# Kernel tuning notes

Hardware: AMD Instinct MI355X
Metric: run time of the kernel (lower is better)

Reference implementation:

```python
import jax, jax.numpy as jnp
import numpy as np

N_HEADS = 16
LN_EPS = 1e-5


def _layer_norm(x, g, b):
    mu = jnp.mean(x, axis=-1, keepdims=True)
    var = jnp.mean(jnp.square(x - mu), axis=-1, keepdims=True)
    return (x - mu) * jax.lax.rsqrt(var + LN_EPS) * g + b


def setup_inputs() -> dict:
    key = jax.random.key(0)
    ks = jax.random.split(key, 6)
    B, S, D = 2, 2048, 1024
    d_ff = 4 * D
    sc = lambda fan_in: 1.0 / np.sqrt(fan_in)
    return {
        "x": jax.random.normal(ks[0], (B, S, D), jnp.float32),
        "in_proj_w": jax.random.normal(ks[1], (3 * D, D), jnp.float32) * sc(D),
        "in_proj_b": jnp.zeros((3 * D,), jnp.float32),
        "out_proj_w": jax.random.normal(ks[2], (D, D), jnp.float32) * sc(D),
        "out_proj_b": jnp.zeros((D,), jnp.float32),
        "ln1_g": jnp.ones((D,), jnp.float32),
        "ln1_b": jnp.zeros((D,), jnp.float32),
        "w1": jax.random.normal(ks[3], (d_ff, D), jnp.float32) * sc(D),
        "b1": jnp.zeros((d_ff,), jnp.float32),
        "w2": jax.random.normal(ks[4], (D, d_ff), jnp.float32) * sc(d_ff),
        "b2": jnp.zeros((D,), jnp.float32),
        "ln2_g": jnp.ones((D,), jnp.float32),
        "ln2_b": jnp.zeros((D,), jnp.float32),
        "window": 128,
    }


def reference(x, in_proj_w, in_proj_b, out_proj_w, out_proj_b,
              ln1_g, ln1_b, w1, b1, w2, b2, ln2_g, ln2_b, window):
    B, S, D = x.shape
    H = N_HEADS
    hd = D // H

    # fused QKV projection (torch Linear convention: x @ W.T + b)
    qkv = x @ in_proj_w.T + in_proj_b            # (B, S, 3D)
    q, k, v = jnp.split(qkv, 3, axis=-1)
    to_heads = lambda t: t.reshape(B, S, H, hd).transpose(0, 2, 1, 3)  # (B,H,S,hd)
    q, k, v = to_heads(q), to_heads(k), to_heads(v)

    scores = jnp.einsum("bhqd,bhkd->bhqk", q, k) / jnp.sqrt(jnp.asarray(hd, x.dtype))
    # banded mask: position i attends to j with |i - j| <= window
    idx = jnp.arange(S)
    band = jnp.abs(idx[:, None] - idx[None, :]) <= window   # (S, S) bool
    scores = jnp.where(band, scores, -jnp.inf)
    probs = jax.nn.softmax(scores, axis=-1)

    attn = jnp.einsum("bhqk,bhkd->bhqd", probs, v)           # (B,H,S,hd)
    attn = attn.transpose(0, 2, 1, 3).reshape(B, S, D)
    attn_out = attn @ out_proj_w.T + out_proj_b

    x2 = _layer_norm(x + attn_out, ln1_g, ln1_b)
    ff = jax.nn.relu(x2 @ w1.T + b1) @ w2.T + b2
    x3 = _layer_norm(x2 + ff, ln2_g, ln2_b)
    return x3
```

## Files before the change

### kernel.cpp

```cpp
#include <hip/hip_runtime.h>
#include <hip/hip_bf16.h>

#define AS1 __attribute__((address_space(1)))
#define AS3 __attribute__((address_space(3)))

typedef __bf16 bf16x8_t __attribute__((ext_vector_type(8)));
typedef float f32x4_t __attribute__((ext_vector_type(4)));
typedef unsigned short ushort_t;
typedef unsigned int uint_t;

static __device__ __forceinline__ ushort_t f2b(float f) {
    __hip_bfloat16 h = __float2bfloat16(f);
    return __builtin_bit_cast(unsigned short, h);
}
static __device__ __forceinline__ float b2f(ushort_t u) {
    return __uint_as_float((uint_t)u << 16);
}

struct CastArgs {
    const float* src[5];
    ushort_t* dst[5];
    int cum[6];
};

__global__ __launch_bounds__(256) void cast_all(CastArgs a) {
    const int i = blockIdx.x * 256 + threadIdx.x;
    if (i >= a.cum[5]) return;
    int s = 0;
#pragma unroll
    for (int k = 1; k < 5; ++k) s += (i >= a.cum[k]);
    const int idx = i - a.cum[s];
    float4 v = ((const float4*)a.src[s])[idx];
    ushort4 o;
    o.x = f2b(v.x); o.y = f2b(v.y); o.z = f2b(v.z); o.w = f2b(v.w);
    ((ushort4*)a.dst[s])[idx] = o;
}

#define EPI_BIAS 1
#define EPI_RELU 2
#define EPI_PART 8
#define EPI_OUTB 16

struct PB { ushort_t* p[4]; };

template <int F>
__global__ __launch_bounds__(256, 2) void gemm_bt(const ushort_t* __restrict__ A,
                                                  const ushort_t* __restrict__ B,
                                                  const float* __restrict__ bias,
                                                  PB pb,
                                                  ushort_t* __restrict__ outb,
                                                  int M, int N, int Kc, int ld) {
    __shared__ ushort_t la[128 * 64];
    __shared__ ushort_t lb[128 * 64];
    const int t = threadIdx.x;

    const int nx = gridDim.x, ny = gridDim.y, nz = gridDim.z;
    const int lid = blockIdx.x + nx * (blockIdx.y + ny * blockIdx.z);
    const int xcd = lid & 7;
    const int slot = lid >> 3;
    const int n_i = slot % nx;
    const int rest = slot / nx;
    const int z = rest % nz;
    const int m_i = xcd * (ny >> 3) + rest / nz;

    const int n0 = n_i * 128;
    const int m0 = m_i * 128;
    const int k0 = z * Kc;
    const int lane = t & 63;
    const int w = t >> 6;
    const int wr = w >> 1, wc = w & 1;
    const int r16 = lane & 15, kq = lane >> 4;

    f32x4_t acc[4][4] = {};

    size_t aoff[4], boff[4];
#pragma unroll
    for (int p = 0; p < 4; ++p) {
        const int c = t + 256 * p;
        const int row = c >> 3, cc = c & 7;
        const int gcol = (cc ^ (row & 7)) * 8;
        aoff[p] = (size_t)(m0 + row) * ld + gcol + k0;
        boff[p] = (size_t)(n0 + row) * ld + gcol + k0;
    }

    for (int kk = 0; kk < Kc; kk += 64) {
#pragma unroll
        for (int p = 0; p < 4; ++p) {
            __builtin_amdgcn_global_load_lds((AS1 void*)(A + aoff[p] + kk),
                                             (AS3 void*)(la + (t + 256 * p) * 8), 16, 0, 0);
            __builtin_amdgcn_global_load_lds((AS1 void*)(B + boff[p] + kk),
                                             (AS3 void*)(lb + (t + 256 * p) * 8), 16, 0, 0);
        }
        __syncthreads();
#pragma unroll
        for (int half = 0; half < 2; ++half) {
            const int sw = ((half * 4 + kq) ^ (r16 & 7)) * 8;
            bf16x8_t af[4], bfr[4];
#pragma unroll
            for (int mi = 0; mi < 4; ++mi)
                af[mi] = *(const bf16x8_t*)(la + (wr * 64 + mi * 16 + r16) * 64 + sw);
#pragma unroll
            for (int ni = 0; ni < 4; ++ni)
                bfr[ni] = *(const bf16x8_t*)(lb + (wc * 64 + ni * 16 + r16) * 64 + sw);
#pragma unroll
            for (int mi = 0; mi < 4; ++mi)
#pragma unroll
                for (int ni = 0; ni < 4; ++ni)
                    acc[mi][ni] = __builtin_amdgcn_mfma_f32_16x16x32_bf16(af[mi], bfr[ni], acc[mi][ni], 0, 0, 0);
        }
        __syncthreads();
    }

    ushort_t* po = (F & EPI_PART) ? pb.p[z] : outb;
#pragma unroll
    for (int mi = 0; mi < 4; ++mi) {
#pragma unroll
        for (int ni = 0; ni < 4; ++ni) {
            const int row = m0 + wr * 64 + mi * 16 + kq * 4;
            const int col = n0 + wc * 64 + ni * 16 + r16;
            float bv = (F & EPI_BIAS) ? bias[col] : 0.f;
#pragma unroll
            for (int i = 0; i < 4; ++i) {
                float v = acc[mi][ni][i] + bv;
                const size_t off = (size_t)(row + i) * N + col;
                if (F & EPI_RELU) v = fmaxf(v, 0.f);
                po[off] = f2b(v);
            }
        }
    }
}

__global__ __launch_bounds__(256, 4) void flash_mfma(const ushort_t* __restrict__ qkv,
                                                     ushort_t* __restrict__ attn) {
    const int S = 2048;
    const int h = blockIdx.y, bb = blockIdx.z;
    const int q0 = blockIdx.x * 64;
    const int t = threadIdx.x;
    const int w = t >> 6, lane = t & 63;
    const int r16 = lane & 15, g = lane >> 4;

    __shared__ ushort_t lk[64 * 72];
    __shared__ ushort_t lv[64 * 68];
    __shared__ ushort_t lp[4 * 16 * 72];

    const ushort_t* base = qkv + (size_t)bb * S * 3072 + (size_t)h * 64;

    bf16x8_t qa[2];
    {
        const ushort_t* qrow = base + (size_t)(q0 + 16 * w + r16) * 3072;
        qa[0] = *(const bf16x8_t*)(qrow + g * 8);
        qa[1] = *(const bf16x8_t*)(qrow + 32 + g * 8);
    }

    f32x4_t O[4] = {};
    float mrow[4] = {-1e30f, -1e30f, -1e30f, -1e30f};
    float lrow[4] = {0.f, 0.f, 0.f, 0.f};

    for (int it = 0; it < 5; ++it) {
        const int kt0 = q0 - 128 + 64 * it;
        if (kt0 < 0 || kt0 >= S) continue;

#pragma unroll
        for (int pass = 0; pass < 2; ++pass) {
            const int c = t + 256 * pass;
            const int key = c >> 3, dc = c & 7;
            const ushort_t* src = base + (size_t)(kt0 + key) * 3072 + dc * 8;
            uint4 kk = *(const uint4*)(src + 1024);
            uint4 vv = *(const uint4*)(src + 2048);
            *(uint4*)(lk + key * 72 + dc * 8) = kk;
            uint2* vd = (uint2*)(lv + key * 68 + dc * 8);
            vd[0] = make_uint2(vv.x, vv.y);
            vd[1] = make_uint2(vv.z, vv.w);
        }
        __syncthreads();

        f32x4_t s[4];
#pragma unroll
        for (int sub = 0; sub < 4; ++sub) {
            const ushort_t* krow = lk + (16 * sub + r16) * 72;
            bf16x8_t kb0 = *(const bf16x8_t*)(krow + g * 8);
            bf16x8_t kb1 = *(const bf16x8_t*)(krow + 32 + g * 8);
            f32x4_t z = {};
            z = __builtin_amdgcn_mfma_f32_16x16x32_bf16(qa[0], kb0, z, 0, 0, 0);
            z = __builtin_amdgcn_mfma_f32_16x16x32_bf16(qa[1], kb1, z, 0, 0, 0);
            s[sub] = z;
        }

        float alpha[4];
#pragma unroll
        for (int reg = 0; reg < 4; ++reg) {
            const int i = q0 + 16 * w + g * 4 + reg;
            float rm = -1e30f;
#pragma unroll
            for (int sub = 0; sub < 4; ++sub) {
                const int j = kt0 + 16 * sub + r16;
                const int d = i - j;
                const bool valid = (d <= 128) && (d >= -128);
                float v = valid ? s[sub][reg] * 0.125f : -1e30f;
                s[sub][reg] = v;
                rm = fmaxf(rm, v);
            }
#pragma unroll
            for (int msk = 1; msk < 16; msk <<= 1) rm = fmaxf(rm, __shfl_xor(rm, msk));
            const float mnew = fmaxf(mrow[reg], rm);
            alpha[reg] = __expf(mrow[reg] - mnew);
            mrow[reg] = mnew;
            float rs = 0.f;
#pragma unroll
            for (int sub = 0; sub < 4; ++sub) {
                float p = __expf(s[sub][reg] - mnew);
                s[sub][reg] = p;
                rs += p;
            }
#pragma unroll
            for (int msk = 1; msk < 16; msk <<= 1) rs += __shfl_xor(rs, msk);
            lrow[reg] = lrow[reg] * alpha[reg] + rs;
#pragma unroll
            for (int dd = 0; dd < 4; ++dd) O[dd][reg] *= alpha[reg];
        }

        ushort_t* pw = lp + w * 16 * 72;
#pragma unroll
        for (int sub = 0; sub < 4; ++sub)
#pragma unroll
            for (int reg = 0; reg < 4; ++reg)
                pw[(g * 4 + reg) * 72 + 16 * sub + r16] = f2b(s[sub][reg]);

        bf16x8_t pa0 = *(const bf16x8_t*)(pw + r16 * 72 + g * 8);
        bf16x8_t pa1 = *(const bf16x8_t*)(pw + r16 * 72 + 32 + g * 8);
        const __bf16* lvb = (const __bf16*)lv;
#pragma unroll
        for (int dd = 0; dd < 4; ++dd) {
            bf16x8_t vb0, vb1;
#pragma unroll
            for (int j = 0; j < 8; ++j) {
                vb0[j] = lvb[(g * 8 + j) * 68 + dd * 16 + r16];
                vb1[j] = lvb[(32 + g * 8 + j) * 68 + dd * 16 + r16];
            }
            O[dd] = __builtin_amdgcn_mfma_f32_16x16x32_bf16(pa0, vb0, O[dd], 0, 0, 0);
            O[dd] = __builtin_amdgcn_mfma_f32_16x16x32_bf16(pa1, vb1, O[dd], 0, 0, 0);
        }
        __syncthreads();
    }

#pragma unroll
    for (int reg = 0; reg < 4; ++reg) {
        const float inv = 1.0f / lrow[reg];
        const int i = q0 + 16 * w + g * 4 + reg;
        ushort_t* orow = attn + ((size_t)(bb * S + i)) * 1024 + (size_t)h * 64;
#pragma unroll
        for (int dd = 0; dd < 4; ++dd)
            orow[dd * 16 + r16] = f2b(O[dd][reg] * inv);
    }
}

template <int NP>
__global__ __launch_bounds__(256) void ln_red(const ushort_t* __restrict__ p0,
                                              const ushort_t* __restrict__ p1,
                                              const ushort_t* __restrict__ p2,
                                              const ushort_t* __restrict__ p3,
                                              const float* __restrict__ bias,
                                              const float* __restrict__ res,
                                              const float* __restrict__ g,
                                              const float* __restrict__ bta,
                                              float* __restrict__ outf,
                                              ushort_t* __restrict__ outb) {
    const int row = blockIdx.x;
    const int t = threadIdx.x;
    const size_t idx = (size_t)row * 256 + t;
    float4 v;
    {
        ushort4 a = ((const ushort4*)p0)[idx];
        ushort4 b = ((const ushort4*)p1)[idx];
        v.x = b2f(a.x) + b2f(b.x);
        v.y = b2f(a.y) + b2f(b.y);
        v.z = b2f(a.z) + b2f(b.z);
        v.w = b2f(a.w) + b2f(b.w);
    }
    if (NP == 4) {
        ushort4 a = ((const ushort4*)p2)[idx];
        ushort4 b = ((const ushort4*)p3)[idx];
        v.x += b2f(a.x) + b2f(b.x);
        v.y += b2f(a.y) + b2f(b.y);
        v.z += b2f(a.z) + b2f(b.z);
        v.w += b2f(a.w) + b2f(b.w);
    }
    {
        float4 bb = ((const float4*)bias)[t];
        float4 rr = ((const float4*)res)[idx];
        v.x += bb.x + rr.x; v.y += bb.y + rr.y; v.z += bb.z + rr.z; v.w += bb.w + rr.w;
    }

    float s = v.x + v.y + v.z + v.w;
    float s2 = v.x * v.x + v.y * v.y + v.z * v.z + v.w * v.w;
#pragma unroll
    for (int off = 32; off > 0; off >>= 1) {
        s += __shfl_down(s, off);
        s2 += __shfl_down(s2, off);
    }
    __shared__ float red[8];
    const int w = t >> 6, lane = t & 63;
    if (lane == 0) { red[w] = s; red[4 + w] = s2; }
    __syncthreads();
    float S1 = red[0] + red[1] + red[2] + red[3];
    float S2 = red[4] + red[5] + red[6] + red[7];
    float mean = S1 * (1.f / 1024.f);
    float var = S2 * (1.f / 1024.f) - mean * mean;
    float r = rsqrtf(var + 1e-5f);
    float4 gg = ((const float4*)g)[t];
    float4 bb = ((const float4*)bta)[t];
    float4 o;
    o.x = (v.x - mean) * r * gg.x + bb.x;
    o.y = (v.y - mean) * r * gg.y + bb.y;
    o.z = (v.z - mean) * r * gg.z + bb.z;
    o.w = (v.w - mean) * r * gg.w + bb.w;
    ((float4*)outf)[idx] = o;
    if (outb) {
        ushort4 ob;
        ob.x = f2b(o.x); ob.y = f2b(o.y); ob.z = f2b(o.z); ob.w = f2b(o.w);
        ((ushort4*)outb)[idx] = ob;
    }
}

extern "C" void kernel_launch(void* const* d_in, const int* in_sizes, int n_in,
                              void* d_out, int out_size, void* d_ws, size_t ws_size,
                              hipStream_t stream) {
    const float* x          = (const float*)d_in[0];
    const float* in_proj_w  = (const float*)d_in[1];
    const float* in_proj_b  = (const float*)d_in[2];
    const float* out_proj_w = (const float*)d_in[3];
    const float* out_proj_b = (const float*)d_in[4];
    const float* ln1_g      = (const float*)d_in[5];
    const float* ln1_b      = (const float*)d_in[6];
    const float* w1         = (const float*)d_in[7];
    const float* b1         = (const float*)d_in[8];
    const float* w2         = (const float*)d_in[9];
    const float* b2         = (const float*)d_in[10];
    const float* ln2_g      = (const float*)d_in[11];
    const float* ln2_b      = (const float*)d_in[12];

    char* ws = (char*)d_ws;
    ushort_t* xb    = (ushort_t*)(ws + (0ull << 20));
    ushort_t* wqkvb = (ushort_t*)(ws + (8ull << 20));
    ushort_t* woutb = (ushort_t*)(ws + (14ull << 20));
    ushort_t* w1b   = (ushort_t*)(ws + (16ull << 20));
    ushort_t* w2b   = (ushort_t*)(ws + (24ull << 20));
    ushort_t* qkvb  = (ushort_t*)(ws + (32ull << 20));
    ushort_t* attnb = (ushort_t*)(ws + (56ull << 20));
    float*    x2f   = (float*)(ws + (80ull << 20));
    ushort_t* x2b   = (ushort_t*)(ws + (96ull << 20));
    ushort_t* hb    = (ushort_t*)(ws + (104ull << 20));
    ushort_t* op_p0 = (ushort_t*)(ws + (64ull << 20));
    ushort_t* op_p1 = (ushort_t*)(ws + (72ull << 20));
    ushort_t* f2_p0 = (ushort_t*)(ws + (0ull << 20));
    ushort_t* f2_p1 = (ushort_t*)(ws + (8ull << 20));
    ushort_t* f2_p2 = (ushort_t*)(ws + (32ull << 20));
    ushort_t* f2_p3 = (ushort_t*)(ws + (40ull << 20));
    (void)in_sizes; (void)n_in; (void)out_size; (void)ws_size;

    CastArgs ca;
    ca.src[0] = x;  ca.dst[0] = xb;
    ca.src[1] = in_proj_w;  ca.dst[1] = wqkvb;
    ca.src[2] = out_proj_w; ca.dst[2] = woutb;
    ca.src[3] = w1; ca.dst[3] = w1b;
    ca.src[4] = w2; ca.dst[4] = w2b;
    ca.cum[0] = 0;
    ca.cum[1] = 1048576;
    ca.cum[2] = 1048576 + 786432;
    ca.cum[3] = 1048576 + 786432 + 262144;
    ca.cum[4] = 1048576 + 786432 + 262144 + 1048576;
    ca.cum[5] = 1048576 + 786432 + 262144 + 1048576 + 1048576;
    cast_all<<<(ca.cum[5] + 255) / 256, 256, 0, stream>>>(ca);

    PB none = {{nullptr, nullptr, nullptr, nullptr}};

    gemm_bt<EPI_BIAS | EPI_OUTB><<<dim3(24, 32, 1), 256, 0, stream>>>(
        xb, wqkvb, in_proj_b, none, qkvb, 4096, 3072, 1024, 1024);

    flash_mfma<<<dim3(32, 16, 2), 256, 0, stream>>>(qkvb, attnb);

    PB op = {{op_p0, op_p1, nullptr, nullptr}};
    gemm_bt<EPI_PART><<<dim3(8, 32, 2), 256, 0, stream>>>(
        attnb, woutb, nullptr, op, nullptr, 4096, 1024, 512, 1024);

    ln_red<2><<<4096, 256, 0, stream>>>(op_p0, op_p1, nullptr, nullptr,
                                        out_proj_b, x, ln1_g, ln1_b, x2f, x2b);

    gemm_bt<EPI_BIAS | EPI_RELU | EPI_OUTB><<<dim3(32, 32, 1), 256, 0, stream>>>(
        x2b, w1b, b1, none, hb, 4096, 4096, 1024, 1024);

    PB f2 = {{f2_p0, f2_p1, f2_p2, f2_p3}};
    gemm_bt<EPI_PART><<<dim3(8, 32, 4), 256, 0, stream>>>(
        hb, w2b, nullptr, f2, nullptr, 4096, 1024, 1024, 4096);

    ln_red<4><<<4096, 256, 0, stream>>>(f2_p0, f2_p1, f2_p2, f2_p3,
                                        b2, x2f, ln2_g, ln2_b, (float*)d_out, nullptr);
}
```

Before: 306.0 us.

## Replace 128x128 GEMM with 256x256 double-buffered pipelined 512-thread GEMM

Swaps the single-buffered 128x128 bf16 GEMM for a 256x256-tile, 8-wave kernel whose LDS holds two K-stages. Global-to-LDS loads for the next tiles are issued between MFMA phases, with explicit vmcnt waits, barriers and setprio. This is meant to hide load latency and raise data reuse per tile. The out-projection split-K also goes from 2 to 4 partials with a matching reduction, and the larger tiles cut the block count, so CU balance may suffer.

```diff
diff --git a/kernel.cpp b/kernel.cpp
--- a/kernel.cpp
+++ b/kernel.cpp
@@ -43,88 +43,121 @@
 
 struct PB { ushort_t* p[4]; };
 
+#define FENCE asm volatile("" ::: "memory")
+
 template <int F>
-__global__ __launch_bounds__(256, 2) void gemm_bt(const ushort_t* __restrict__ A,
+__global__ __launch_bounds__(512, 2) void gemm256(const ushort_t* __restrict__ A,
                                                   const ushort_t* __restrict__ B,
                                                   const float* __restrict__ bias,
                                                   PB pb,
                                                   ushort_t* __restrict__ outb,
                                                   int M, int N, int Kc, int ld) {
-    __shared__ ushort_t la[128 * 64];
-    __shared__ ushort_t lb[128 * 64];
+    __shared__ __align__(16) ushort_t lds[8 * 8192];
     const int t = threadIdx.x;
 
     const int nx = gridDim.x, ny = gridDim.y, nz = gridDim.z;
     const int lid = blockIdx.x + nx * (blockIdx.y + ny * blockIdx.z);
-    const int xcd = lid & 7;
-    const int slot = lid >> 3;
+    const int xcd = lid & 7, slot = lid >> 3;
     const int n_i = slot % nx;
     const int rest = slot / nx;
     const int z = rest % nz;
     const int m_i = xcd * (ny >> 3) + rest / nz;
 
-    const int n0 = n_i * 128;
-    const int m0 = m_i * 128;
-    const int k0 = z * Kc;
-    const int lane = t & 63;
-    const int w = t >> 6;
-    const int wr = w >> 1, wc = w & 1;
+    const int n0 = n_i * 256, m0 = m_i * 256, k0 = z * Kc;
+    const int lane = t & 63, w = t >> 6;
+    const int wr = w >> 2, wc = w & 3;
     const int r16 = lane & 15, kq = lane >> 4;
-
-    f32x4_t acc[4][4] = {};
-
-    size_t aoff[4], boff[4];
-#pragma unroll
-    for (int p = 0; p < 4; ++p) {
-        const int c = t + 256 * p;
-        const int row = c >> 3, cc = c & 7;
-        const int gcol = (cc ^ (row & 7)) * 8;
-        aoff[p] = (size_t)(m0 + row) * ld + gcol + k0;
-        boff[p] = (size_t)(n0 + row) * ld + gcol + k0;
-    }
-
-    for (int kk = 0; kk < Kc; kk += 64) {
-#pragma unroll
-        for (int p = 0; p < 4; ++p) {
-            __builtin_amdgcn_global_load_lds((AS1 void*)(A + aoff[p] + kk),
-                                             (AS3 void*)(la + (t + 256 * p) * 8), 16, 0, 0);
-            __builtin_amdgcn_global_load_lds((AS1 void*)(B + boff[p] + kk),
-                                             (AS3 void*)(lb + (t + 256 * p) * 8), 16, 0, 0);
-        }
-        __syncthreads();
-#pragma unroll
-        for (int half = 0; half < 2; ++half) {
-            const int sw = ((half * 4 + kq) ^ (r16 & 7)) * 8;
-            bf16x8_t af[4], bfr[4];
+    const int NT = Kc >> 6;
+
+    f32x4_t acc[8][4] = {};
+
+    const int srow = t >> 2;
+    const int gq = (t & 3) ^ ((t >> 3) & 3);
+    const ushort_t* ag = A + (size_t)(m0 + srow) * ld + gq * 8 + k0;
+    const ushort_t* bg = B + (size_t)(n0 + srow) * ld + gq * 8 + k0;
+    const size_t step2 = (size_t)128 * ld;
+
+    auto stage = [&](const ushort_t* g, int buf, int ab, int kk, int Tt) {
+        const ushort_t* s = g + Tt * 64 + kk * 32;
+        ushort_t* d = lds + ((buf * 2 + ab) * 2 + kk) * 8192 + t * 8;
+        __builtin_amdgcn_global_load_lds((AS1 void*)s, (AS3 void*)d, 16, 0, 0);
+        __builtin_amdgcn_global_load_lds((AS1 void*)(s + step2), (AS3 void*)(d + 4096), 16, 0, 0);
+    };
+
+    stage(ag, 0, 0, 0, 0);
+    stage(bg, 0, 1, 0, 0);
+    stage(ag, 0, 0, 1, 0);
+    stage(bg, 0, 1, 1, 0);
+    stage(ag, 1, 0, 0, 1);
+    stage(bg, 1, 1, 0, 1);
+    asm volatile("s_waitcnt vmcnt(8)" ::: "memory");
+    FENCE;
+    __builtin_amdgcn_s_barrier();
+    FENCE;
+
+    const int ccA = (kq ^ ((r16 >> 1) & 3)) * 8;
+    bf16x8_t bfr[4];
+
+    for (int T = 0; T < NT; ++T) {
+        const int buf = T & 1;
+        const ushort_t* pa[2]  = { lds + ((buf * 2 + 0) * 2 + 0) * 8192,
+                                   lds + ((buf * 2 + 0) * 2 + 1) * 8192 };
+        const ushort_t* pbB[2] = { lds + ((buf * 2 + 1) * 2 + 0) * 8192,
+                                   lds + ((buf * 2 + 1) * 2 + 1) * 8192 };
+#pragma unroll
+        for (int ph = 0; ph < 4; ++ph) {
+            const int mh = ph & 1, kk = ph >> 1;
+            bf16x8_t af[4];
 #pragma unroll
             for (int mi = 0; mi < 4; ++mi)
-                af[mi] = *(const bf16x8_t*)(la + (wr * 64 + mi * 16 + r16) * 64 + sw);
-#pragma unroll
-            for (int ni = 0; ni < 4; ++ni)
-                bfr[ni] = *(const bf16x8_t*)(lb + (wc * 64 + ni * 16 + r16) * 64 + sw);
+                af[mi] = *(const bf16x8_t*)(pa[kk] + (wr * 128 + mh * 64 + mi * 16 + r16) * 32 + ccA);
+            if (mh == 0) {
+#pragma unroll
+                for (int ni = 0; ni < 4; ++ni)
+                    bfr[ni] = *(const bf16x8_t*)(pbB[kk] + (wc * 64 + ni * 16 + r16) * 32 + ccA);
+            }
+            if (ph == 0 && T + 1 < NT) stage(ag, buf ^ 1, 0, 1, T + 1);
+            if (ph == 1 && T + 1 < NT) stage(bg, buf ^ 1, 1, 1, T + 1);
+            if (ph == 2 && T + 2 < NT) stage(ag, buf, 0, 0, T + 2);
+            if (ph == 3 && T + 2 < NT) stage(bg, buf, 1, 0, T + 2);
+            FENCE;
+            __builtin_amdgcn_s_barrier();
+            asm volatile("s_waitcnt lgkmcnt(0)" ::: "memory");
+            __builtin_amdgcn_sched_barrier(0);
+            __builtin_amdgcn_s_setprio(1);
 #pragma unroll
             for (int mi = 0; mi < 4; ++mi)
 #pragma unroll
                 for (int ni = 0; ni < 4; ++ni)
-                    acc[mi][ni] = __builtin_amdgcn_mfma_f32_16x16x32_bf16(af[mi], bfr[ni], acc[mi][ni], 0, 0, 0);
-        }
-        __syncthreads();
+                    acc[mh * 4 + mi][ni] = __builtin_amdgcn_mfma_f32_16x16x32_bf16(
+                        af[mi], bfr[ni], acc[mh * 4 + mi][ni], 0, 0, 0);
+            __builtin_amdgcn_s_setprio(0);
+            if (ph == 1) {
+                if (T < NT - 1) { asm volatile("s_waitcnt vmcnt(8)" ::: "memory"); }
+                else            { asm volatile("s_waitcnt vmcnt(0)" ::: "memory"); }
+            } else if (ph == 3) {
+                if (T < NT - 2)       { asm volatile("s_waitcnt vmcnt(8)" ::: "memory"); }
+                else if (T == NT - 2) { asm volatile("s_waitcnt vmcnt(4)" ::: "memory"); }
+            }
+            FENCE;
+            __builtin_amdgcn_s_barrier();
+            FENCE;
+        }
     }
 
     ushort_t* po = (F & EPI_PART) ? pb.p[z] : outb;
 #pragma unroll
-    for (int mi = 0; mi < 4; ++mi) {
+    for (int a = 0; a < 8; ++a) {
 #pragma unroll
         for (int ni = 0; ni < 4; ++ni) {
-            const int row = m0 + wr * 64 + mi * 16 + kq * 4;
+            const int row = m0 + wr * 128 + a * 16 + kq * 4;
             const int col = n0 + wc * 64 + ni * 16 + r16;
             float bv = (F & EPI_BIAS) ? bias[col] : 0.f;
 #pragma unroll
             for (int i = 0; i < 4; ++i) {
-                float v = acc[mi][ni][i] + bv;
-                const size_t off = (size_t)(row + i) * N + col;
+                float v = acc[a][ni][i] + bv;
                 if (F & EPI_RELU) v = fmaxf(v, 0.f);
-                po[off] = f2b(v);
+                po[(size_t)(row + i) * N + col] = f2b(v);
             }
         }
     }
@@ -352,6 +385,8 @@
     ushort_t* hb    = (ushort_t*)(ws + (104ull << 20));
     ushort_t* op_p0 = (ushort_t*)(ws + (64ull << 20));
     ushort_t* op_p1 = (ushort_t*)(ws + (72ull << 20));
+    ushort_t* op_p2 = (ushort_t*)(ws + (112ull << 20));
+    ushort_t* op_p3 = (ushort_t*)(ws + (120ull << 20));
     ushort_t* f2_p0 = (ushort_t*)(ws + (0ull << 20));
     ushort_t* f2_p1 = (ushort_t*)(ws + (8ull << 20));
     ushort_t* f2_p2 = (ushort_t*)(ws + (32ull << 20));
@@ -374,23 +409,23 @@
 
     PB none = {{nullptr, nullptr, nullptr, nullptr}};
 
-    gemm_bt<EPI_BIAS | EPI_OUTB><<<dim3(24, 32, 1), 256, 0, stream>>>(
+    gemm256<EPI_BIAS | EPI_OUTB><<<dim3(12, 16, 1), 512, 0, stream>>>(
         xb, wqkvb, in_proj_b, none, qkvb, 4096, 3072, 1024, 1024);
 
     flash_mfma<<<dim3(32, 16, 2), 256, 0, stream>>>(qkvb, attnb);
 
-    PB op = {{op_p0, op_p1, nullptr, nullptr}};
-    gemm_bt<EPI_PART><<<dim3(8, 32, 2), 256, 0, stream>>>(
-        attnb, woutb, nullptr, op, nullptr, 4096, 1024, 512, 1024);
-
-    ln_red<2><<<4096, 256, 0, stream>>>(op_p0, op_p1, nullptr, nullptr,
+    PB op = {{op_p0, op_p1, op_p2, op_p3}};
+    gemm256<EPI_PART><<<dim3(4, 16, 4), 512, 0, stream>>>(
+        attnb, woutb, nullptr, op, nullptr, 4096, 1024, 256, 1024);
+
+    ln_red<4><<<4096, 256, 0, stream>>>(op_p0, op_p1, op_p2, op_p3,
                                         out_proj_b, x, ln1_g, ln1_b, x2f, x2b);
 
-    gemm_bt<EPI_BIAS | EPI_RELU | EPI_OUTB><<<dim3(32, 32, 1), 256, 0, stream>>>(
+    gemm256<EPI_BIAS | EPI_RELU | EPI_OUTB><<<dim3(16, 16, 1), 512, 0, stream>>>(
         x2b, w1b, b1, none, hb, 4096, 4096, 1024, 1024);
 
     PB f2 = {{f2_p0, f2_p1, f2_p2, f2_p3}};
-    gemm_bt<EPI_PART><<<dim3(8, 32, 4), 256, 0, stream>>>(
+    gemm256<EPI_PART><<<dim3(4, 16, 4), 512, 0, stream>>>(
         hb, w2b, nullptr, f2, nullptr, 4096, 1024, 1024, 4096);
 
     ln_red<4><<<4096, 256, 0, stream>>>(f2_p0, f2_p1, f2_p2, f2_p3,
```

Result: no change. 307.9 us (+0.6%).

## Merge all stages into one persistent megakernel with software grid barriers

Applied to the files above, without the earlier changes.

Replaces the seven separate launches (cast, QKV GEMM, attention, out-proj GEMM, LN1, FFN GEMMs, LN2) with one persistent kernel of 512 blocks. The blocks loop over each stage's tiles and separate stages with an atomic-counter grid barrier. The aim is to remove launch overhead and inter-kernel gaps. In exchange, every stage must fit one launch shape and one shared-memory budget, a grid-wide sync is paid at each stage boundary, and the barrier relies on all 512 blocks being co-resident. If that does not hold it can deadlock, and the fallback places the barrier counters in the output buffer's tail.

```diff
diff --git a/kernel.cpp b/kernel.cpp
--- a/kernel.cpp
+++ b/kernel.cpp
@@ -17,45 +17,49 @@
     return __uint_as_float((uint_t)u << 16);
 }
 
-struct CastArgs {
-    const float* src[5];
-    ushort_t* dst[5];
-    int cum[6];
-};
-
-__global__ __launch_bounds__(256) void cast_all(CastArgs a) {
-    const int i = blockIdx.x * 256 + threadIdx.x;
-    if (i >= a.cum[5]) return;
-    int s = 0;
-#pragma unroll
-    for (int k = 1; k < 5; ++k) s += (i >= a.cum[k]);
-    const int idx = i - a.cum[s];
-    float4 v = ((const float4*)a.src[s])[idx];
-    ushort4 o;
-    o.x = f2b(v.x); o.y = f2b(v.y); o.z = f2b(v.z); o.w = f2b(v.w);
-    ((ushort4*)a.dst[s])[idx] = o;
-}
-
 #define EPI_BIAS 1
 #define EPI_RELU 2
 #define EPI_PART 8
 #define EPI_OUTB 16
 
-struct PB { ushort_t* p[4]; };
+static __device__ __forceinline__ void gsync(uint_t* cnt, uint_t* gen, uint_t nb) {
+    __syncthreads();
+    if (threadIdx.x == 0) {
+        __threadfence();
+        uint_t g = atomicAdd(gen, 0u);
+        if (atomicAdd(cnt, 1u) == nb - 1u) {
+            __threadfence();
+            atomicExch(cnt, 0u);
+            __threadfence();
+            atomicAdd(gen, 1u);
+        } else {
+            while (atomicAdd(gen, 0u) == g) __builtin_amdgcn_s_sleep(8);
+        }
+        __threadfence();
+    }
+    __syncthreads();
+}
+
+static __device__ __forceinline__ void cast_arr(const float* __restrict__ src,
+                                                ushort_t* __restrict__ dst,
+                                                int n4, int tid, int nthr) {
+    for (int i = tid; i < n4; i += nthr) {
+        float4 v = ((const float4*)src)[i];
+        ushort4 o;
+        o.x = f2b(v.x); o.y = f2b(v.y); o.z = f2b(v.z); o.w = f2b(v.w);
+        ((ushort4*)dst)[i] = o;
+    }
+}
 
 template <int F>
-__global__ __launch_bounds__(256, 2) void gemm_bt(const ushort_t* __restrict__ A,
-                                                  const ushort_t* __restrict__ B,
-                                                  const float* __restrict__ bias,
-                                                  PB pb,
-                                                  ushort_t* __restrict__ outb,
-                                                  int M, int N, int Kc, int ld) {
-    __shared__ ushort_t la[128 * 64];
-    __shared__ ushort_t lb[128 * 64];
-    const int t = threadIdx.x;
-
-    const int nx = gridDim.x, ny = gridDim.y, nz = gridDim.z;
-    const int lid = blockIdx.x + nx * (blockIdx.y + ny * blockIdx.z);
+static __device__ void gemm_tile(ushort_t* la, ushort_t* lb,
+                                 const ushort_t* __restrict__ A,
+                                 const ushort_t* __restrict__ B,
+                                 const float* __restrict__ bias,
+                                 ushort_t* p0, ushort_t* p1, ushort_t* p2, ushort_t* p3,
+                                 ushort_t* __restrict__ outb,
+                                 int N, int Kc, int ld,
+                                 int lid, int nx, int ny, int nz, int t) {
     const int xcd = lid & 7;
     const int slot = lid >> 3;
     const int n_i = slot % nx;
@@ -111,7 +115,14 @@
         __syncthreads();
     }
 
-    ushort_t* po = (F & EPI_PART) ? pb.p[z] : outb;
+    ushort_t* po;
+    if (F & EPI_PART) {
+        ushort_t* lo = (z & 1) ? p1 : p0;
+        ushort_t* hi = (z & 1) ? p3 : p2;
+        po = (z & 2) ? hi : lo;
+    } else {
+        po = outb;
+    }
 #pragma unroll
     for (int mi = 0; mi < 4; ++mi) {
 #pragma unroll
@@ -130,18 +141,15 @@
     }
 }
 
-__global__ __launch_bounds__(256, 4) void flash_mfma(const ushort_t* __restrict__ qkv,
-                                                     ushort_t* __restrict__ attn) {
+static __device__ void flash_tile(ushort_t* lk, ushort_t* lv, ushort_t* lp,
+                                  const ushort_t* __restrict__ qkv,
+                                  ushort_t* __restrict__ attn,
+                                  int lid, int t) {
     const int S = 2048;
-    const int h = blockIdx.y, bb = blockIdx.z;
-    const int q0 = blockIdx.x * 64;
-    const int t = threadIdx.x;
+    const int h = (lid >> 5) & 15, bb = lid >> 9;
+    const int q0 = (lid & 31) * 64;
     const int w = t >> 6, lane = t & 63;
     const int r16 = lane & 15, g = lane >> 4;
-
-    __shared__ ushort_t lk[64 * 72];
-    __shared__ ushort_t lv[64 * 68];
-    __shared__ ushort_t lp[4 * 16 * 72];
 
     const ushort_t* base = qkv + (size_t)bb * S * 3072 + (size_t)h * 64;
 
@@ -255,18 +263,18 @@
 }
 
 template <int NP>
-__global__ __launch_bounds__(256) void ln_red(const ushort_t* __restrict__ p0,
-                                              const ushort_t* __restrict__ p1,
-                                              const ushort_t* __restrict__ p2,
-                                              const ushort_t* __restrict__ p3,
-                                              const float* __restrict__ bias,
-                                              const float* __restrict__ res,
-                                              const float* __restrict__ g,
-                                              const float* __restrict__ bta,
-                                              float* __restrict__ outf,
-                                              ushort_t* __restrict__ outb) {
-    const int row = blockIdx.x;
-    const int t = threadIdx.x;
+static __device__ void ln_row(float* red,
+                              const ushort_t* __restrict__ p0,
+                              const ushort_t* __restrict__ p1,
+                              const ushort_t* __restrict__ p2,
+                              const ushort_t* __restrict__ p3,
+                              const float* __restrict__ bias,
+                              const float* __restrict__ res,
+                              const float* __restrict__ g,
+                              const float* __restrict__ bta,
+                              float* __restrict__ outf,
+                              ushort_t* __restrict__ outb,
+                              int row, int t) {
     const size_t idx = (size_t)row * 256 + t;
     float4 v;
     {
@@ -298,7 +306,6 @@
         s += __shfl_down(s, off);
         s2 += __shfl_down(s2, off);
     }
-    __shared__ float red[8];
     const int w = t >> 6, lane = t & 63;
     if (lane == 0) { red[w] = s; red[4 + w] = s2; }
     __syncthreads();
@@ -320,79 +327,115 @@
         ob.x = f2b(o.x); ob.y = f2b(o.y); ob.z = f2b(o.z); ob.w = f2b(o.w);
         ((ushort4*)outb)[idx] = ob;
     }
+    __syncthreads();
+}
+
+struct MegaArgs {
+    const float *x, *in_proj_w, *in_proj_b, *out_proj_w, *out_proj_b;
+    const float *ln1_g, *ln1_b, *w1, *b1, *w2, *b2, *ln2_g, *ln2_b;
+    ushort_t *xb, *wqkvb, *woutb, *w1b, *w2b, *qkvb, *attnb, *x2b, *hb;
+    float *x2f, *outf;
+    ushort_t *op_p0, *op_p1, *f2_p0, *f2_p1, *f2_p2, *f2_p3;
+    uint_t *bcnt, *bgen;
+};
+
+__global__ __launch_bounds__(256, 2) void mega(MegaArgs a) {
+    __shared__ __align__(16) ushort_t smem[16384];
+    const int t = threadIdx.x;
+    const int nb = gridDim.x;
+    const int tid = blockIdx.x * 256 + t;
+    const int nthr = nb * 256;
+
+    cast_arr(a.x,          a.xb,    1048576, tid, nthr);
+    cast_arr(a.in_proj_w,  a.wqkvb,  786432, tid, nthr);
+    cast_arr(a.out_proj_w, a.woutb,  262144, tid, nthr);
+    cast_arr(a.w1,         a.w1b,   1048576, tid, nthr);
+    cast_arr(a.w2,         a.w2b,   1048576, tid, nthr);
+    gsync(a.bcnt, a.bgen, nb);
+
+    for (int lid = blockIdx.x; lid < 768; lid += nb)
+        gemm_tile<EPI_BIAS | EPI_OUTB>(smem, smem + 8192, a.xb, a.wqkvb, a.in_proj_b,
+                                       nullptr, nullptr, nullptr, nullptr, a.qkvb,
+                                       3072, 1024, 1024, lid, 24, 32, 1, t);
+    gsync(a.bcnt, a.bgen, nb);
+
+    for (int lid = blockIdx.x; lid < 1024; lid += nb)
+        flash_tile(smem, smem + 4608, smem + 8960, a.qkvb, a.attnb, lid, t);
+    gsync(a.bcnt, a.bgen, nb);
+
+    for (int lid = blockIdx.x; lid < 512; lid += nb)
+        gemm_tile<EPI_PART>(smem, smem + 8192, a.attnb, a.woutb, nullptr,
+                            a.op_p0, a.op_p1, nullptr, nullptr, nullptr,
+                            1024, 512, 1024, lid, 8, 32, 2, t);
+    gsync(a.bcnt, a.bgen, nb);
+
+    for (int row = blockIdx.x; row < 4096; row += nb)
+        ln_row<2>((float*)smem, a.op_p0, a.op_p1, nullptr, nullptr,
+                  a.out_proj_b, a.x, a.ln1_g, a.ln1_b, a.x2f, a.x2b, row, t);
+    gsync(a.bcnt, a.bgen, nb);
+
+    for (int lid = blockIdx.x; lid < 1024; lid += nb)
+        gemm_tile<EPI_BIAS | EPI_RELU | EPI_OUTB>(smem, smem + 8192, a.x2b, a.w1b, a.b1,
+                                                  nullptr, nullptr, nullptr, nullptr, a.hb,
+                                                  4096, 1024, 1024, lid, 32, 32, 1, t);
+    gsync(a.bcnt, a.bgen, nb);
+
+    for (int lid = blockIdx.x; lid < 1024; lid += nb)
+        gemm_tile<EPI_PART>(smem, smem + 8192, a.hb, a.w2b, nullptr,
+                            a.f2_p0, a.f2_p1, a.f2_p2, a.f2_p3, nullptr,
+                            1024, 1024, 4096, lid, 8, 32, 4, t);
+    gsync(a.bcnt, a.bgen, nb);
+
+    for (int row = blockIdx.x; row < 4096; row += nb)
+        ln_row<4>((float*)smem, a.f2_p0, a.f2_p1, a.f2_p2, a.f2_p3,
+                  a.b2, a.x2f, a.ln2_g, a.ln2_b, a.outf, nullptr, row, t);
 }
 
 extern "C" void kernel_launch(void* const* d_in, const int* in_sizes, int n_in,
                               void* d_out, int out_size, void* d_ws, size_t ws_size,
                               hipStream_t stream) {
-    const float* x          = (const float*)d_in[0];
-    const float* in_proj_w  = (const float*)d_in[1];
-    const float* in_proj_b  = (const float*)d_in[2];
-    const float* out_proj_w = (const float*)d_in[3];
-    const float* out_proj_b = (const float*)d_in[4];
-    const float* ln1_g      = (const float*)d_in[5];
-    const float* ln1_b      = (const float*)d_in[6];
-    const float* w1         = (const float*)d_in[7];
-    const float* b1         = (const float*)d_in[8];
-    const float* w2         = (const float*)d_in[9];
-    const float* b2         = (const float*)d_in[10];
-    const float* ln2_g      = (const float*)d_in[11];
-    const float* ln2_b      = (const float*)d_in[12];
-
     char* ws = (char*)d_ws;
-    ushort_t* xb    = (ushort_t*)(ws + (0ull << 20));
-    ushort_t* wqkvb = (ushort_t*)(ws + (8ull << 20));
-    ushort_t* woutb = (ushort_t*)(ws + (14ull << 20));
-    ushort_t* w1b   = (ushort_t*)(ws + (16ull << 20));
-    ushort_t* w2b   = (ushort_t*)(ws + (24ull << 20));
-    ushort_t* qkvb  = (ushort_t*)(ws + (32ull << 20));
-    ushort_t* attnb = (ushort_t*)(ws + (56ull << 20));
-    float*    x2f   = (float*)(ws + (80ull << 20));
-    ushort_t* x2b   = (ushort_t*)(ws + (96ull << 20));
-    ushort_t* hb    = (ushort_t*)(ws + (104ull << 20));
-    ushort_t* op_p0 = (ushort_t*)(ws + (64ull << 20));
-    ushort_t* op_p1 = (ushort_t*)(ws + (72ull << 20));
-    ushort_t* f2_p0 = (ushort_t*)(ws + (0ull << 20));
-    ushort_t* f2_p1 = (ushort_t*)(ws + (8ull << 20));
-    ushort_t* f2_p2 = (ushort_t*)(ws + (32ull << 20));
-    ushort_t* f2_p3 = (ushort_t*)(ws + (40ull << 20));
-    (void)in_sizes; (void)n_in; (void)out_size; (void)ws_size;
-
-    CastArgs ca;
-    ca.src[0] = x;  ca.dst[0] = xb;
-    ca.src[1] = in_proj_w;  ca.dst[1] = wqkvb;
-    ca.src[2] = out_proj_w; ca.dst[2] = woutb;
-    ca.src[3] = w1; ca.dst[3] = w1b;
-    ca.src[4] = w2; ca.dst[4] = w2b;
-    ca.cum[0] = 0;
-    ca.cum[1] = 1048576;
-    ca.cum[2] = 1048576 + 786432;
-    ca.cum[3] = 1048576 + 786432 + 262144;
-    ca.cum[4] = 1048576 + 786432 + 262144 + 1048576;
-    ca.cum[5] = 1048576 + 786432 + 262144 + 1048576 + 1048576;
-    cast_all<<<(ca.cum[5] + 255) / 256, 256, 0, stream>>>(ca);
-
-    PB none = {{nullptr, nullptr, nullptr, nullptr}};
-
-    gemm_bt<EPI_BIAS | EPI_OUTB><<<dim3(24, 32, 1), 256, 0, stream>>>(
-        xb, wqkvb, in_proj_b, none, qkvb, 4096, 3072, 1024, 1024);
-
-    flash_mfma<<<dim3(32, 16, 2), 256, 0, stream>>>(qkvb, attnb);
-
-    PB op = {{op_p0, op_p1, nullptr, nullptr}};
-    gemm_bt<EPI_PART><<<dim3(8, 32, 2), 256, 0, stream>>>(
-        attnb, woutb, nullptr, op, nullptr, 4096, 1024, 512, 1024);
-
-    ln_red<2><<<4096, 256, 0, stream>>>(op_p0, op_p1, nullptr, nullptr,
-                                        out_proj_b, x, ln1_g, ln1_b, x2f, x2b);
-
-    gemm_bt<EPI_BIAS | EPI_RELU | EPI_OUTB><<<dim3(32, 32, 1), 256, 0, stream>>>(
-        x2b, w1b, b1, none, hb, 4096, 4096, 1024, 1024);
-
-    PB f2 = {{f2_p0, f2_p1, f2_p2, f2_p3}};
-    gemm_bt<EPI_PART><<<dim3(8, 32, 4), 256, 0, stream>>>(
-        hb, w2b, nullptr, f2, nullptr, 4096, 1024, 1024, 4096);
-
-    ln_red<4><<<4096, 256, 0, stream>>>(f2_p0, f2_p1, f2_p2, f2_p3,
-                                        b2, x2f, ln2_g, ln2_b, (float*)d_out, nullptr);
-}
+    MegaArgs a;
+    a.x          = (const float*)d_in[0];
+    a.in_proj_w  = (const float*)d_in[1];
+    a.in_proj_b  = (const float*)d_in[2];
+    a.out_proj_w = (const float*)d_in[3];
+    a.out_proj_b = (const float*)d_in[4];
+    a.ln1_g      = (const float*)d_in[5];
+    a.ln1_b      = (const float*)d_in[6];
+    a.w1         = (const float*)d_in[7];
+    a.b1         = (const float*)d_in[8];
+    a.w2         = (const float*)d_in[9];
+    a.b2         = (const float*)d_in[10];
+    a.ln2_g      = (const float*)d_in[11];
+    a.ln2_b      = (const float*)d_in[12];
+
+    a.xb    = (ushort_t*)(ws + (0ull << 20));
+    a.wqkvb = (ushort_t*)(ws + (8ull << 20));
+    a.woutb = (ushort_t*)(ws + (14ull << 20));
+    a.w1b   = (ushort_t*)(ws + (16ull << 20));
+    a.w2b   = (ushort_t*)(ws + (24ull << 20));
+    a.qkvb  = (ushort_t*)(ws + (32ull << 20));
+    a.attnb = (ushort_t*)(ws + (56ull << 20));
+    a.x2f   = (float*)(ws + (80ull << 20));
+    a.x2b   = (ushort_t*)(ws + (96ull << 20));
+    a.hb    = (ushort_t*)(ws + (104ull << 20));
+    a.op_p0 = (ushort_t*)(ws + (64ull << 20));
+    a.op_p1 = (ushort_t*)(ws + (72ull << 20));
+    a.f2_p0 = (ushort_t*)(ws + (0ull << 20));
+    a.f2_p1 = (ushort_t*)(ws + (8ull << 20));
+    a.f2_p2 = (ushort_t*)(ws + (32ull << 20));
+    a.f2_p3 = (ushort_t*)(ws + (40ull << 20));
+    a.outf  = (float*)d_out;
+
+    uint_t* bar;
+    if (ws_size >= (137ull << 20)) bar = (uint_t*)(ws + (136ull << 20));
+    else bar = (uint_t*)((char*)d_out + 16ull * 1024 * 1024 - 64);
+    a.bcnt = bar;
+    a.bgen = bar + 1;
+    hipMemsetAsync(bar, 0, 8, stream);
+
+    (void)in_sizes; (void)n_in; (void)out_size;
+
+    hipLaunchKernelGGL(mega, dim3(512), dim3(256), 0, stream, a);
+}
```

Result: slower. 737.9 us (+141.2%).
